# Kernel tuning notes

Hardware: AMD Instinct MI355X
Metric: run time of the kernel (lower is better)

Reference implementation:

```python
import jax, jax.numpy as jnp
import numpy as np

DIM = 1024
HEADS = 8
HD = DIM // HEADS          # 128
HALF = HD // 2             # 64 complex pairs
EPS = 1e-6
T, L, H, W = 10, 4, 21, 37
TOK_PER_FRAME = 1 + L * (5 + H * W)   # 3129
SK = T * TOK_PER_FRAME                # 31290
SQ = 512
THETA = 10000.0


def _inv_freqs(dim):
    # matches precompute_freqs_cis: 1/theta**(arange(0,dim,2)/dim)
    return 1.0 / THETA ** (np.arange(0, dim, 2)[: dim // 2].astype(np.float64) / dim)


def _angles(t_idx, h_idx, w_idx):
    # 3D RoPE split per precompute_freqs_cis_3d: f gets HD-2*(HD//3)=44 dims, h/w get HD//3=42 each
    hd3 = HD // 3
    inv_f = _inv_freqs(HD - 2 * hd3)  # 22 freqs
    inv_h = _inv_freqs(hd3)           # 21 freqs
    inv_w = _inv_freqs(hd3)           # 21 freqs
    ang = np.concatenate([
        t_idx[:, None] * inv_f[None, :],
        h_idx[:, None] * inv_h[None, :],
        w_idx[:, None] * inv_w[None, :],
    ], axis=-1)  # [S, 64]
    return ang


def _memory_positions():
    # per-frame layout from build_3d_freqs_unified: 1 pose token (h=w=0),
    # then per layer: 5 register tokens (h=w=0) + H*W grid tokens
    h_f, w_f = [0], [0]
    grid_h, grid_w = np.meshgrid(np.arange(H), np.arange(W), indexing='ij')
    for _ in range(L):
        h_f += [0] * 5 + list(grid_h.ravel())
        w_f += [0] * 5 + list(grid_w.ravel())
    h_f = np.asarray(h_f, np.float64)
    w_f = np.asarray(w_f, np.float64)
    t_idx = np.repeat(np.arange(T, dtype=np.float64), TOK_PER_FRAME)
    return t_idx, np.tile(h_f, T), np.tile(w_f, T)


def setup_inputs() -> dict:
    key = jax.random.key(0)
    ks = jax.random.split(key, 8)
    # RoPE angle tables
    tq = np.zeros(SQ)  # use_time_encoding=False for queries -> t=0
    hq = (np.arange(SQ) // W) % H
    wq = np.arange(SQ) % W
    ang_q = _angles(tq.astype(np.float64), hq.astype(np.float64), wq.astype(np.float64))
    tk, hk, wk = _memory_positions()
    ang_k = _angles(tk, hk, wk)
    s = 0.02
    inp = {
        'x': jax.random.normal(ks[0], (1, SQ, DIM), jnp.float32),
        'mem': jax.random.normal(ks[1], (1, SK, DIM), jnp.float32),
        'mask': jax.random.randint(ks[2], (1, SK), 0, 2) > 0,
        'cos_q': jnp.asarray(np.cos(ang_q), jnp.float32),
        'sin_q': jnp.asarray(np.sin(ang_q), jnp.float32),
        'cos_k': jnp.asarray(np.cos(ang_k), jnp.float32),
        'sin_k': jnp.asarray(np.sin(ang_k), jnp.float32),
        'Wq': jax.random.normal(ks[3], (DIM, DIM), jnp.float32) * s,
        'bq': jnp.zeros((DIM,), jnp.float32),
        'Wk': jax.random.normal(ks[4], (DIM, DIM), jnp.float32) * s,
        'bk': jnp.zeros((DIM,), jnp.float32),
        'Wv': jax.random.normal(ks[5], (DIM, DIM), jnp.float32) * s,
        'bv': jnp.zeros((DIM,), jnp.float32),
        'Wo': jax.random.normal(ks[6], (DIM, DIM), jnp.float32) * s,
        'bo': jnp.zeros((DIM,), jnp.float32),
        'gq': jnp.ones((DIM,), jnp.float32),
        'gk': jnp.ones((DIM,), jnp.float32),
    }
    return inp


def _rmsnorm(x, g):
    xf = x.astype(jnp.float32)
    y = xf * jax.lax.rsqrt(jnp.mean(xf * xf, axis=-1, keepdims=True) + EPS)
    return y.astype(x.dtype) * g


def _rope(x, cos, sin):
    # x: [B,S,D]; complex rotation on interleaved pairs per head, freqs shared across heads
    B, S, _ = x.shape
    xh = x.reshape(B, S, HEADS, HALF, 2)
    xr, xi = xh[..., 0], xh[..., 1]
    c = cos[None, :, None, :]
    s = sin[None, :, None, :]
    orr = xr * c - xi * s
    oi = xr * s + xi * c
    return jnp.stack([orr, oi], axis=-1).reshape(B, S, HEADS * HD)


def reference(x, mem, mask, cos_q, sin_q, cos_k, sin_k,
              Wq, bq, Wk, bk, Wv, bv, Wo, bo, gq, gk):
    q = _rmsnorm(x @ Wq.T + bq, gq)
    k = _rmsnorm(mem @ Wk.T + bk, gk)
    v = mem @ Wv.T + bv
    q = _rope(q, cos_q, sin_q)
    k = _rope(k, cos_k, sin_k)
    B, Sq, _ = q.shape
    Sk = k.shape[1]
    qh = q.reshape(B, Sq, HEADS, HD)
    kh = k.reshape(B, Sk, HEADS, HD)
    vh = v.reshape(B, Sk, HEADS, HD)
    scores = jnp.einsum('bqnd,bknd->bnqk', qh, kh) / jnp.sqrt(jnp.float32(HD))
    bias = jnp.where(mask[:, None, None, :], 0.0, -jnp.inf).astype(scores.dtype)
    attn = jax.nn.softmax(scores + bias, axis=-1)
    out = jnp.einsum('bnqk,bknd->bqnd', attn, vh).reshape(B, Sq, DIM)
    return out @ Wo.T + bo
```

## Files before the change

kernel.cpp:

```cpp
#include <hip/hip_runtime.h>
#include <cstdint>

typedef __bf16 bf16;
typedef __bf16 bf16x8 __attribute__((ext_vector_type(8)));
typedef __bf16 bf16x4 __attribute__((ext_vector_type(4)));
typedef float f32x4 __attribute__((ext_vector_type(4)));

#define DEVINL __device__ __forceinline__

namespace {
constexpr int DIM = 1024, HEADS = 8, HD = 128, HALF = 64;
constexpr int SQ = 512;
constexpr int SK = 31290;
constexpr int SKP = 31488;
constexpr int NSPLIT = 24;

constexpr long OFF_MEMB = 0;
constexpr long OFF_XB   = OFF_MEMB + (long)SKP * DIM * 2;
constexpr long OFF_WKV  = OFF_XB + (long)SQ * DIM * 2;
constexpr long OFF_WQ   = OFF_WKV + 2048L * DIM * 2;
constexpr long OFF_WO   = OFF_WQ + (long)DIM * DIM * 2;
constexpr long OFF_BKV  = OFF_WO + (long)DIM * DIM * 2;
constexpr long OFF_KPRE = OFF_BKV + 2048L * 4;
constexpr long OFF_VT   = OFF_KPRE + (long)SKP * DIM * 2;
constexpr long OFF_QPRE = OFF_VT + (long)DIM * SKP * 2;
constexpr long OFF_QR   = OFF_QPRE + (long)SQ * DIM * 4;
constexpr long OFF_BIAS = OFF_QR + (long)SQ * DIM * 2;
constexpr long OFF_ML   = OFF_BIAS + (long)SKP * 4;
constexpr long OFF_AO   = OFF_ML + (long)NSPLIT * HEADS * SQ * 2 * 4;
constexpr long OFF_IDX  = OFF_AO + (long)SQ * DIM * 2;
constexpr long OFF_NKC  = OFF_IDX + 31744L * 4;
constexpr long OFF_OP   = OFF_MEMB;
}

DEVINL void gl_lds16(const void* g, void* l) {
  __builtin_amdgcn_global_load_lds(
      (__attribute__((address_space(1))) void*)(void*)g,
      (__attribute__((address_space(3))) void*)l, 16, 0, 0);
}


__global__ __launch_bounds__(1024) void k_scan(const int* __restrict__ mask,
                                               int* __restrict__ idx,
                                               int* __restrict__ nkcp) {
  int tid = threadIdx.x, lane = tid & 63, wv = tid >> 6;
  __shared__ int wsum[16];
  __shared__ int base;
  if (tid == 0) base = 0;
  __syncthreads();
  for (int c = 0; c < 31; ++c) {
    int i = c * 1024 + tid;
    int m = (i < SK) ? (mask[i] != 0) : 0;
    unsigned long long bal = __ballot(m);
    int wpre = (int)__popcll(bal & ((1ull << lane) - 1ull));
    if (lane == 0) wsum[wv] = (int)__popcll(bal);
    __syncthreads();
    int woff = 0;
    #pragma unroll
    for (int j = 0; j < 16; ++j) woff += (j < wv) ? wsum[j] : 0;
    if (m) idx[base + woff + wpre] = i;
    __syncthreads();
    if (tid == 0) {
      int tot = 0;
      #pragma unroll
      for (int j = 0; j < 16; ++j) tot += wsum[j];
      base += tot;
    }
    __syncthreads();
  }
  if (tid == 0) *nkcp = base;
}


__global__ __launch_bounds__(256) void k_cvt_mem(const float* __restrict__ mem,
                                                 const int* __restrict__ idx,
                                                 const int* __restrict__ nkcp,
                                                 bf16* __restrict__ memb,
                                                 float* __restrict__ biasA) {
  long i = (long)blockIdx.x * 256 + threadIdx.x;
  long e = i * 8;
  if (e >= (long)SKP * DIM) return;
  int row = (int)(e >> 10);
  int nkc = *nkcp;
  int lim = ((((nkc + 63) & ~63) + 255) & ~255);
  if (row >= lim) return;
  if ((e & 1023) == 0) biasA[row] = (row < nkc) ? 0.0f : -1e30f;
  bf16x8 o;
  if (row < nkc) {
    long se = ((long)idx[row] << 10) + (e & 1023);
    float4 a = *(const float4*)(mem + se);
    float4 b = *(const float4*)(mem + se + 4);
    o[0] = (bf16)a.x; o[1] = (bf16)a.y; o[2] = (bf16)a.z; o[3] = (bf16)a.w;
    o[4] = (bf16)b.x; o[5] = (bf16)b.y; o[6] = (bf16)b.z; o[7] = (bf16)b.w;
  } else {
    #pragma unroll
    for (int j = 0; j < 8; ++j) o[j] = (bf16)0.0f;
  }
  *(bf16x8*)(memb + e) = o;
}

__global__ __launch_bounds__(256) void k_prep(const float* __restrict__ x,
    const float* __restrict__ Wq, const float* __restrict__ Wo,
    const float* __restrict__ Wk, const float* __restrict__ Wv,
    const float* __restrict__ bk, const float* __restrict__ bv,
    bf16* __restrict__ xb, bf16* __restrict__ WqB, bf16* __restrict__ WoB,
    bf16* __restrict__ WkvB, float* __restrict__ bKV) {
  long i = (long)blockIdx.x * 256 + threadIdx.x;
  constexpr long n_x = 65536, n_w = 131072;
  const float* src;
  bf16* dst;
  long off;
  if (i < n_x) { src = x; dst = xb; off = i; }
  else if (i < n_x + n_w) { src = Wq; dst = WqB; off = i - n_x; }
  else if (i < n_x + 2 * n_w) { src = Wo; dst = WoB; off = i - n_x - n_w; }
  else if (i < n_x + 2 * n_w + 262144) {
    long j = i - n_x - 2 * n_w;
    long e = j * 8;
    int n = (int)(e >> 10);
    const float* s2 = (n < 1024) ? (Wk + e) : (Wv + e - 1024L * 1024);
    float4 a = *(const float4*)(s2);
    float4 b = *(const float4*)(s2 + 4);
    bf16x8 o;
    o[0] = (bf16)a.x; o[1] = (bf16)a.y; o[2] = (bf16)a.z; o[3] = (bf16)a.w;
    o[4] = (bf16)b.x; o[5] = (bf16)b.y; o[6] = (bf16)b.z; o[7] = (bf16)b.w;
    *(bf16x8*)(WkvB + e) = o;
    if (j < 2048) bKV[j] = (j < 1024) ? bk[j] : bv[j - 1024];
    return;
  } else return;
  long e = off * 8;
  float4 a = *(const float4*)(src + e);
  float4 b = *(const float4*)(src + e + 4);
  bf16x8 o;
  o[0] = (bf16)a.x; o[1] = (bf16)a.y; o[2] = (bf16)a.z; o[3] = (bf16)a.w;
  o[4] = (bf16)b.x; o[5] = (bf16)b.y; o[6] = (bf16)b.z; o[7] = (bf16)b.w;
  *(bf16x8*)(dst + e) = o;
}


template<int MODE>
__global__ __launch_bounds__(256, 2)
void k_gemm(const bf16* __restrict__ A, const bf16* __restrict__ B,
            const float* __restrict__ bias, int Mtiles, int Ntiles,
            float* __restrict__ outF, int ldF,
            bf16* __restrict__ outK, bf16* __restrict__ outVT) {
  constexpr int K = 1024;
  __shared__ char lds[32768];
  char* ldsA = lds;
  char* ldsB = lds + 16384;
  int tid = threadIdx.x;
  int w = tid >> 6, lane = tid & 63;
  int cpx = gridDim.x >> 3;
  int bid = (blockIdx.x & 7) * cpx + (blockIdx.x >> 3);
  int mt = bid / Ntiles, nt = bid % Ntiles;
  int m0 = mt * 128, n0 = nt * 128;
  int wm = w >> 1, wn = w & 1;
  int cl = lane & 15, rg = lane >> 4;

  f32x4 acc[4][4] = {};

  int rowi = lane >> 3, g = lane & 7;
  for (int kt = 0; kt < K / 64; ++kt) {
    #pragma unroll
    for (int j = 0; j < 4; ++j) {
      int rb = (w * 4 + j) * 8;
      int row = rb + rowi;
      int gs = g ^ (row & 7);
      gl_lds16((const char*)(A + (long)(m0 + row) * K + kt * 64) + gs * 16, ldsA + rb * 128);
      gl_lds16((const char*)(B + (long)(n0 + row) * K + kt * 64) + gs * 16, ldsB + rb * 128);
    }
    __syncthreads();
    #pragma unroll
    for (int ks = 0; ks < 2; ++ks) {
      bf16x8 af[4], bfr[4];
      #pragma unroll
      for (int i = 0; i < 4; ++i) {
        int rowA = wm * 64 + i * 16 + cl;
        int c = ks * 4 + rg;
        af[i] = *(const bf16x8*)(ldsA + rowA * 128 + ((c ^ (rowA & 7)) * 16));
        int rowB = wn * 64 + i * 16 + cl;
        bfr[i] = *(const bf16x8*)(ldsB + rowB * 128 + ((c ^ (rowB & 7)) * 16));
      }
      #pragma unroll
      for (int mf = 0; mf < 4; ++mf)
        #pragma unroll
        for (int nf = 0; nf < 4; ++nf)
          acc[mf][nf] = __builtin_amdgcn_mfma_f32_16x16x32_bf16(af[mf], bfr[nf], acc[mf][nf], 0, 0, 0);
    }
    __syncthreads();
  }

  #pragma unroll
  for (int mf = 0; mf < 4; ++mf) {
    #pragma unroll
    for (int nf = 0; nf < 4; ++nf) {
      int n = n0 + wn * 64 + nf * 16 + cl;
      float bval = bias[n];
      int mb = m0 + wm * 64 + mf * 16 + rg * 4;
      #pragma unroll
      for (int rr = 0; rr < 4; ++rr)
        outF[(long)(mb + rr) * ldF + n] = acc[mf][nf][rr] + bval;
    }
  }
}


#define KV_PHASE(P)                                                                   \
  {                                                                                   \
    bf16x8 a00 = dsA(cur, 2 * (P), 0),     a01 = dsA(cur, 2 * (P), 1);                \
    bf16x8 a10 = dsA(cur, 2 * (P) + 1, 0), a11 = dsA(cur, 2 * (P) + 1, 1);            \
    __builtin_amdgcn_s_setprio(1);                                                    \
    _Pragma("unroll")                                                                 \
    for (int nf = 0; nf < 4; ++nf) {                                                  \
      acc[2 * (P)][nf]     = __builtin_amdgcn_mfma_f32_16x16x32_bf16(a00, bb[nf][0], acc[2 * (P)][nf], 0, 0, 0);     \
      acc[2 * (P) + 1][nf] = __builtin_amdgcn_mfma_f32_16x16x32_bf16(a10, bb[nf][0], acc[2 * (P) + 1][nf], 0, 0, 0); \
    }                                                                                 \
    _Pragma("unroll")                                                                 \
    for (int nf = 0; nf < 4; ++nf) {                                                  \
      acc[2 * (P)][nf]     = __builtin_amdgcn_mfma_f32_16x16x32_bf16(a01, bb[nf][1], acc[2 * (P)][nf], 0, 0, 0);     \
      acc[2 * (P) + 1][nf] = __builtin_amdgcn_mfma_f32_16x16x32_bf16(a11, bb[nf][1], acc[2 * (P) + 1][nf], 0, 0, 0); \
    }                                                                                 \
    __builtin_amdgcn_s_setprio(0);                                                    \
  }

__global__ __launch_bounds__(512)
void k_gemm_kv(const bf16* __restrict__ A, const bf16* __restrict__ B,
               const float* __restrict__ bias, const int* __restrict__ nkcp,
               bf16* __restrict__ outK, bf16* __restrict__ outVT) {
  constexpr int K = 1024, NTK = 16;
  __shared__ char lds[131072];
  const int tid = threadIdx.x;
  const int w = tid >> 6, lane = tid & 63;
  const int mt = blockIdx.x >> 3, nt = blockIdx.x & 7;
  const int m0 = mt * 256, n0 = nt * 256;
  if (m0 >= ((*nkcp + 63) & ~63)) return;
  const int wm = w >> 2, wn = w & 3;
  const int cl = lane & 15, rg = lane >> 4;
  const int srow = lane >> 3, sg = lane & 7;

  f32x4 acc[8][4] = {};

  auto stage = [&](int b, int kt, int isB, int cr) {
    const bf16* src = isB ? B : A;
    int r = cr + w * 8 + srow;
    int gs = sg ^ (r & 7);
    const char* gp = (const char*)(src + (long)((isB ? n0 : m0) + r) * K + kt * 64) + gs * 16;
    char* lp = lds + b * 65536 + isB * 32768 + (cr + w * 8) * 128;
    gl_lds16(gp, lp);
  };
  auto dsA = [&](int b, int mf, int ks) -> bf16x8 {
    int r = wm * 128 + mf * 16 + cl;
    int c = ks * 4 + rg;
    return *(const bf16x8*)(lds + b * 65536 + r * 128 + ((c ^ (r & 7)) * 16));
  };
  auto dsB = [&](int b, int nf, int ks) -> bf16x8 {
    int r = wn * 64 + nf * 16 + cl;
    int c = ks * 4 + rg;
    return *(const bf16x8*)(lds + b * 65536 + 32768 + r * 128 + ((c ^ (r & 7)) * 16));
  };

  stage(0, 0, 1, 0);   stage(0, 0, 1, 64);
  stage(0, 0, 1, 128); stage(0, 0, 1, 192);
  stage(0, 0, 0, 0);   stage(0, 0, 0, 128);
  stage(0, 0, 0, 64);  stage(0, 0, 0, 192);

  for (int t = 0; t < NTK; ++t) {
    const int cur = t & 1, nxt = cur ^ 1;
    const bool pre = (t + 1 < NTK);
    bf16x8 bb[4][2];

    if (pre) {
      stage(nxt, t + 1, 1, 0); stage(nxt, t + 1, 1, 64);
      asm volatile("s_waitcnt vmcnt(4)\ns_barrier" ::: "memory");
    } else {
      asm volatile("s_waitcnt vmcnt(2)\ns_barrier" ::: "memory");
    }
    #pragma unroll
    for (int nf = 0; nf < 4; ++nf) { bb[nf][0] = dsB(cur, nf, 0); bb[nf][1] = dsB(cur, nf, 1); }
    KV_PHASE(0)
    asm volatile("s_barrier" ::: "memory");
    if (pre) { stage(nxt, t + 1, 1, 128); stage(nxt, t + 1, 1, 192); }
    KV_PHASE(1)
    asm volatile("s_barrier" ::: "memory");
    if (pre) {
      stage(nxt, t + 1, 0, 0); stage(nxt, t + 1, 0, 128);
      asm volatile("s_waitcnt vmcnt(6)\ns_barrier" ::: "memory");
    } else {
      asm volatile("s_waitcnt vmcnt(0)\ns_barrier" ::: "memory");
    }
    KV_PHASE(2)
    asm volatile("s_barrier" ::: "memory");
    if (pre) { stage(nxt, t + 1, 0, 64); stage(nxt, t + 1, 0, 192); }
    KV_PHASE(3)
    asm volatile("s_barrier" ::: "memory");
  }

  if (nt < 4) {
    #pragma unroll
    for (int mf = 0; mf < 8; ++mf)
      #pragma unroll
      for (int nf = 0; nf < 4; ++nf) {
        int n = n0 + wn * 64 + nf * 16 + cl;
        float bval = bias[n];
        int mrow = m0 + wm * 128 + mf * 16 + rg * 4;
        #pragma unroll
        for (int rr = 0; rr < 4; ++rr)
          outK[(long)(mrow + rr) * 1024 + n] = (bf16)(acc[mf][nf][rr] + bval);
      }
  } else {
    #pragma unroll
    for (int mf = 0; mf < 8; ++mf)
      #pragma unroll
      for (int nf = 0; nf < 4; ++nf) {
        int n = n0 + wn * 64 + nf * 16 + cl;
        float bval = bias[n];
        int mrow = m0 + wm * 128 + mf * 16 + rg * 4;
        bf16x4 pk;
        #pragma unroll
        for (int rr = 0; rr < 4; ++rr) pk[rr] = (bf16)(acc[mf][nf][rr] + bval);
        *(bf16x4*)(outVT + (long)(n - 1024) * SKP + mrow) = pk;
      }
  }
}


__global__ __launch_bounds__(256) void k_fuse_q(const float* __restrict__ QP,
    bf16* __restrict__ Qr, const float* __restrict__ gg,
    const float* __restrict__ cosT, const float* __restrict__ sinT) {
  int row = blockIdx.x, tid = threadIdx.x;
  int d0 = tid * 4;
  float4 t = *(const float4*)(QP + (long)row * DIM + d0);
  float v0 = t.x, v1 = t.y, v2 = t.z, v3 = t.w;
  float ss = v0 * v0 + v1 * v1 + v2 * v2 + v3 * v3;
  #pragma unroll
  for (int m = 1; m < 64; m <<= 1) ss += __shfl_xor(ss, m);
  __shared__ float red[4];
  if ((tid & 63) == 0) red[tid >> 6] = ss;
  __syncthreads();
  float rn = rsqrtf((red[0] + red[1] + red[2] + red[3]) * (1.0f / DIM) + 1e-6f);
  v0 *= rn * gg[d0]; v1 *= rn * gg[d0 + 1]; v2 *= rn * gg[d0 + 2]; v3 *= rn * gg[d0 + 3];
  int i0 = (d0 & 127) >> 1;
  float c0 = cosT[(long)row * HALF + i0], s0 = sinT[(long)row * HALF + i0];
  float c1 = cosT[(long)row * HALF + i0 + 1], s1 = sinT[(long)row * HALF + i0 + 1];
  bf16x4 o = { (bf16)(v0 * c0 - v1 * s0), (bf16)(v0 * s0 + v1 * c0),
               (bf16)(v2 * c1 - v3 * s1), (bf16)(v2 * s1 + v3 * c1) };
  *(bf16x4*)(Qr + (long)row * DIM + d0) = o;
}

__global__ __launch_bounds__(256) void k_fuse_k(bf16* __restrict__ KP,
    const float* __restrict__ gg, const float* __restrict__ cosT,
    const float* __restrict__ sinT, const int* __restrict__ idx,
    const int* __restrict__ nkcp) {
  int row = blockIdx.x, tid = threadIdx.x;
  int nkc = *nkcp;
  if (row >= ((nkc + 63) & ~63)) return;
  int orig = (row < nkc) ? idx[row] : 0;
  int d0 = tid * 4;
  bf16x4 t = *(const bf16x4*)(KP + (long)row * DIM + d0);
  float v0 = (float)t[0], v1 = (float)t[1], v2 = (float)t[2], v3 = (float)t[3];
  float ss = v0 * v0 + v1 * v1 + v2 * v2 + v3 * v3;
  #pragma unroll
  for (int m = 1; m < 64; m <<= 1) ss += __shfl_xor(ss, m);
  __shared__ float red[4];
  if ((tid & 63) == 0) red[tid >> 6] = ss;
  __syncthreads();
  float rn = rsqrtf((red[0] + red[1] + red[2] + red[3]) * (1.0f / DIM) + 1e-6f);
  v0 *= rn * gg[d0]; v1 *= rn * gg[d0 + 1]; v2 *= rn * gg[d0 + 2]; v3 *= rn * gg[d0 + 3];
  int i0 = (d0 & 127) >> 1;
  float c0 = cosT[(long)orig * HALF + i0], s0 = sinT[(long)orig * HALF + i0];
  float c1 = cosT[(long)orig * HALF + i0 + 1], s1 = sinT[(long)orig * HALF + i0 + 1];
  bf16x4 o = { (bf16)(v0 * c0 - v1 * s0), (bf16)(v0 * s0 + v1 * c0),
               (bf16)(v2 * c1 - v3 * s1), (bf16)(v2 * s1 + v3 * c1) };
  *(bf16x4*)(KP + (long)row * DIM + d0) = o;
}


__global__ __launch_bounds__(256, 2)
void k_attn(const bf16* __restrict__ Kr, const bf16* __restrict__ VT,
            const bf16* __restrict__ Qr, const float* __restrict__ biasA,
            const int* __restrict__ nkcp,
            float* __restrict__ Opart, float* __restrict__ ml) {
  __shared__ char lds[49152];
  char* ldsK = lds;
  char* ldsV = lds + 16384;
  int tid = threadIdx.x, w = tid >> 6, lane = tid & 63;
  char* ldsP = lds + 32768 + w * 4096;
  int bid = blockIdx.x;
  int swz = (bid & 7) * 96 + (bid >> 3);
  int sp = swz >> 5, h = (swz >> 2) & 7, qb = swz & 3;
  int NTC = (*nkcp + 63) >> 6;
  int t0 = (sp * NTC) / NSPLIT;
  int t1 = ((sp + 1) * NTC) / NSPLIT;
  int cl = lane & 15, rg = lane >> 4;
  int qbase = qb * 128 + w * 32;

  bf16x8 qf[2][4];
  #pragma unroll
  for (int mf = 0; mf < 2; ++mf)
    #pragma unroll
    for (int ks = 0; ks < 4; ++ks)
      qf[mf][ks] = *(const bf16x8*)(Qr + (long)(qbase + mf * 16 + cl) * DIM + h * HD + ks * 32 + rg * 8);

  bf16x8 ones;
  #pragma unroll
  for (int j = 0; j < 8; ++j) ones[j] = (bf16)1.0f;

  f32x4 Oa[2][8] = {};
  f32x4 l_acc[2] = {};
  float m_r[2] = {-1e30f, -1e30f};

  const float sc = 0.08838834764831845f;
  for (int t = t0; t < t1; ++t) {
    int k0 = t * 64;
    __syncthreads();
    {
      int rK = lane >> 4, gK = lane & 15;
      #pragma unroll
      for (int j = 0; j < 4; ++j) {
        int rb = w * 16 + j * 4;
        int row = rb + rK;
        int gs = gK ^ (row & 7);
        gl_lds16((const char*)(Kr + (long)(k0 + row) * DIM + h * HD) + gs * 16,
                 ldsK + rb * 256);
      }
      int rV = lane >> 3, gV = lane & 7;
      #pragma unroll
      for (int j = 0; j < 4; ++j) {
        int db = w * 32 + j * 8;
        int d = db + rV;
        int gs = gV ^ (d & 7);
        gl_lds16((const char*)(VT + (long)(h * HD + d) * SKP + k0) + gs * 16,
                 ldsV + db * 128);
      }
    }
    __syncthreads();

    f32x4 sa[2][4] = {};
    #pragma unroll
    for (int ks = 0; ks < 4; ++ks) {
      #pragma unroll
      for (int nf = 0; nf < 4; ++nf) {
        int key = nf * 16 + cl;
        int c = ks * 4 + rg;
        bf16x8 kb = *(const bf16x8*)(ldsK + key * 256 + ((c ^ (key & 7)) * 16));
        sa[0][nf] = __builtin_amdgcn_mfma_f32_16x16x32_bf16(qf[0][ks], kb, sa[0][nf], 0, 0, 0);
        sa[1][nf] = __builtin_amdgcn_mfma_f32_16x16x32_bf16(qf[1][ks], kb, sa[1][nf], 0, 0, 0);
      }
    }

    float bia[4];
    #pragma unroll
    for (int nf = 0; nf < 4; ++nf) bia[nf] = biasA[k0 + nf * 16 + cl];

    #pragma unroll
    for (int mf = 0; mf < 2; ++mf) {
      char* ldsPmf = ldsP + mf * 2048;
      #pragma unroll
      for (int nf = 0; nf < 4; ++nf)
        #pragma unroll
        for (int r = 0; r < 4; ++r) sa[mf][nf][r] = sa[mf][nf][r] * sc + bia[nf];
      float mx = sa[mf][0][0];
      #pragma unroll
      for (int nf = 0; nf < 4; ++nf)
        #pragma unroll
        for (int r = 0; r < 4; ++r) mx = fmaxf(mx, sa[mf][nf][r]);
      mx = fmaxf(mx, __shfl_xor(mx, 1));
      mx = fmaxf(mx, __shfl_xor(mx, 2));
      mx = fmaxf(mx, __shfl_xor(mx, 4));
      mx = fmaxf(mx, __shfl_xor(mx, 8));
      bool grew = mx > m_r[mf] + 6.0f;
      if (__any(grew)) {
        float mn = grew ? mx : m_r[mf];
        float scale = __expf(m_r[mf] - mn);
        m_r[mf] = mn;
        l_acc[mf] *= scale;
        #pragma unroll
        for (int df = 0; df < 8; ++df) Oa[mf][df] *= scale;
      }
      #pragma unroll
      for (int nf = 0; nf < 4; ++nf)
        #pragma unroll
        for (int r = 0; r < 4; ++r) {
          float p = __expf(sa[mf][nf][r] - m_r[mf]);
          int qr = rg * 4 + r;
          int col = nf * 16 + cl;
          int gp = (col >> 3) ^ (qr & 7);
          *(bf16*)(ldsPmf + qr * 128 + gp * 16 + (col & 7) * 2) = (bf16)p;
        }
    }

    #pragma unroll
    for (int ks = 0; ks < 2; ++ks) {
      int c = ks * 4 + rg;
      bf16x8 pa0 = *(const bf16x8*)(ldsP + cl * 128 + ((c ^ (cl & 7)) * 16));
      bf16x8 pa1 = *(const bf16x8*)(ldsP + 2048 + cl * 128 + ((c ^ (cl & 7)) * 16));
      l_acc[0] = __builtin_amdgcn_mfma_f32_16x16x32_bf16(pa0, ones, l_acc[0], 0, 0, 0);
      l_acc[1] = __builtin_amdgcn_mfma_f32_16x16x32_bf16(pa1, ones, l_acc[1], 0, 0, 0);
      #pragma unroll
      for (int df = 0; df < 8; ++df) {
        int d = df * 16 + cl;
        bf16x8 vb = *(const bf16x8*)(ldsV + d * 128 + ((c ^ (d & 7)) * 16));
        Oa[0][df] = __builtin_amdgcn_mfma_f32_16x16x32_bf16(pa0, vb, Oa[0][df], 0, 0, 0);
        Oa[1][df] = __builtin_amdgcn_mfma_f32_16x16x32_bf16(pa1, vb, Oa[1][df], 0, 0, 0);
      }
    }
  }

  long rowb = (long)(sp * HEADS + h) * SQ + qbase;
  #pragma unroll
  for (int mf = 0; mf < 2; ++mf) {
    #pragma unroll
    for (int df = 0; df < 8; ++df)
      #pragma unroll
      for (int r = 0; r < 4; ++r) {
        int qr = mf * 16 + rg * 4 + r;
        Opart[(rowb + qr) * HD + df * 16 + cl] = Oa[mf][df][r];
      }
    if (cl == 0) {
      #pragma unroll
      for (int r = 0; r < 4; ++r) {
        int qr = mf * 16 + rg * 4 + r;
        ml[(rowb + qr) * 2] = m_r[mf];
        ml[(rowb + qr) * 2 + 1] = l_acc[mf][r];
      }
    }
  }
}

__global__ __launch_bounds__(128) void k_combine(const float* __restrict__ Opart,
    const float* __restrict__ ml, bf16* __restrict__ AO) {
  int bid = blockIdx.x;
  int h = bid >> 9, qq = bid & 511;
  int d = threadIdx.x;
  float M = -1e30f;
  #pragma unroll 4
  for (int s2 = 0; s2 < NSPLIT; ++s2) {
    long mi = (long)(s2 * HEADS + h) * SQ + qq;
    M = fmaxf(M, ml[mi * 2]);
  }
  float L = 0.f, acc = 0.f;
  #pragma unroll 4
  for (int s2 = 0; s2 < NSPLIT; ++s2) {
    long mi = (long)(s2 * HEADS + h) * SQ + qq;
    float wgt = __expf(ml[mi * 2] - M);
    L += wgt * ml[mi * 2 + 1];
    acc += wgt * Opart[mi * HD + d];
  }
  AO[(long)qq * DIM + h * HD + d] = (bf16)(acc / L);
}


extern "C" void kernel_launch(void* const* d_in, const int* in_sizes, int n_in,
                              void* d_out, int out_size, void* d_ws, size_t ws_size,
                              hipStream_t stream) {
  const float* x     = (const float*)d_in[0];
  const float* mem   = (const float*)d_in[1];
  const int*   mask  = (const int*)d_in[2];
  const float* cos_q = (const float*)d_in[3];
  const float* sin_q = (const float*)d_in[4];
  const float* cos_k = (const float*)d_in[5];
  const float* sin_k = (const float*)d_in[6];
  const float* Wq    = (const float*)d_in[7];
  const float* bq    = (const float*)d_in[8];
  const float* Wk    = (const float*)d_in[9];
  const float* bk    = (const float*)d_in[10];
  const float* Wv    = (const float*)d_in[11];
  const float* bv    = (const float*)d_in[12];
  const float* Wo    = (const float*)d_in[13];
  const float* bo    = (const float*)d_in[14];
  const float* gq    = (const float*)d_in[15];
  const float* gk    = (const float*)d_in[16];

  char* ws = (char*)d_ws;
  bf16*  memb = (bf16*)(ws + OFF_MEMB);
  bf16*  xb   = (bf16*)(ws + OFF_XB);
  bf16*  WkvB = (bf16*)(ws + OFF_WKV);
  bf16*  WqB  = (bf16*)(ws + OFF_WQ);
  bf16*  WoB  = (bf16*)(ws + OFF_WO);
  float* bKV  = (float*)(ws + OFF_BKV);
  bf16*  Kpre = (bf16*)(ws + OFF_KPRE);
  bf16*  VT   = (bf16*)(ws + OFF_VT);
  float* Qpre = (float*)(ws + OFF_QPRE);
  bf16*  Qr   = (bf16*)(ws + OFF_QR);
  float* biasA= (float*)(ws + OFF_BIAS);
  float* Opart= (float*)(ws + OFF_OP);
  float* mlb  = (float*)(ws + OFF_ML);
  bf16*  AO   = (bf16*)(ws + OFF_AO);
  int*   idx  = (int*)(ws + OFF_IDX);
  int*   nkcp = (int*)(ws + OFF_NKC);

  k_scan<<<dim3(1), dim3(1024), 0, stream>>>(mask, idx, nkcp);
  k_cvt_mem<<<dim3(SKP * DIM / 8 / 256), dim3(256), 0, stream>>>(mem, idx, nkcp, memb, biasA);
  k_prep<<<dim3(2304), dim3(256), 0, stream>>>(x, Wq, Wo, Wk, Wv, bk, bv,
                                               xb, WqB, WoB, WkvB, bKV);

  k_gemm<0><<<dim3(4 * 8), dim3(256), 0, stream>>>(xb, WqB, bq, 4, 8, Qpre, DIM,
                                                   (bf16*)nullptr, (bf16*)nullptr);
  k_gemm_kv<<<dim3(984), dim3(512), 0, stream>>>(memb, WkvB, bKV, nkcp, Kpre, VT);

  k_fuse_q<<<dim3(SQ), dim3(256), 0, stream>>>(Qpre, Qr, gq, cos_q, sin_q);
  k_fuse_k<<<dim3(SKP), dim3(256), 0, stream>>>(Kpre, gk, cos_k, sin_k, idx, nkcp);

  k_attn<<<dim3(NSPLIT * HEADS * 4), dim3(256), 0, stream>>>(Kpre, VT, Qr, biasA, nkcp, Opart, mlb);
  k_combine<<<dim3(HEADS * SQ), dim3(128), 0, stream>>>(Opart, mlb, AO);

  k_gemm<0><<<dim3(4 * 8), dim3(256), 0, stream>>>(AO, WoB, bo, 4, 8, (float*)d_out, DIM,
                                                   (bf16*)nullptr, (bf16*)nullptr);
  (void)in_sizes; (void)n_in; (void)out_size; (void)ws_size;
}
```

Measured before the change: 257.1 us.

## Transpose QK MFMA so softmax rows are lane-local; drop bias buffer and ones-MFMA

The score MFMA now has its operands swapped so each lane holds keys for a fixed query, which cuts the row max/sum reductions to two cross-lane shuffles instead of four. The row sum is accumulated in registers, which removes the extra MFMA against a vector of ones. The key mask is computed inline from nkc, so the bias buffer and its global loads go away. Each P tile is stored in row-major LDS with a 144-byte padded stride instead of an XOR swizzle. In exchange, rescaling the output accumulator now needs per-row scale shuffles, and LDS use per block grows slightly.

```diff
diff --git a/kernel.cpp b/kernel.cpp
--- a/kernel.cpp
+++ b/kernel.cpp
@@ -25,8 +25,7 @@
 constexpr long OFF_VT   = OFF_KPRE + (long)SKP * DIM * 2;
 constexpr long OFF_QPRE = OFF_VT + (long)DIM * SKP * 2;
 constexpr long OFF_QR   = OFF_QPRE + (long)SQ * DIM * 4;
-constexpr long OFF_BIAS = OFF_QR + (long)SQ * DIM * 2;
-constexpr long OFF_ML   = OFF_BIAS + (long)SKP * 4;
+constexpr long OFF_ML   = OFF_QR + (long)SQ * DIM * 2;
 constexpr long OFF_AO   = OFF_ML + (long)NSPLIT * HEADS * SQ * 2 * 4;
 constexpr long OFF_IDX  = OFF_AO + (long)SQ * DIM * 2;
 constexpr long OFF_NKC  = OFF_IDX + 31744L * 4;
@@ -75,8 +74,7 @@
 __global__ __launch_bounds__(256) void k_cvt_mem(const float* __restrict__ mem,
                                                  const int* __restrict__ idx,
                                                  const int* __restrict__ nkcp,
-                                                 bf16* __restrict__ memb,
-                                                 float* __restrict__ biasA) {
+                                                 bf16* __restrict__ memb) {
   long i = (long)blockIdx.x * 256 + threadIdx.x;
   long e = i * 8;
   if (e >= (long)SKP * DIM) return;
@@ -84,7 +82,6 @@
   int nkc = *nkcp;
   int lim = ((((nkc + 63) & ~63) + 255) & ~255);
   if (row >= lim) return;
-  if ((e & 1023) == 0) biasA[row] = (row < nkc) ? 0.0f : -1e30f;
   bf16x8 o;
   if (row < nkc) {
     long se = ((long)idx[row] << 10) + (e & 1023);
@@ -376,18 +373,18 @@
 
 __global__ __launch_bounds__(256, 2)
 void k_attn(const bf16* __restrict__ Kr, const bf16* __restrict__ VT,
-            const bf16* __restrict__ Qr, const float* __restrict__ biasA,
-            const int* __restrict__ nkcp,
+            const bf16* __restrict__ Qr, const int* __restrict__ nkcp,
             float* __restrict__ Opart, float* __restrict__ ml) {
-  __shared__ char lds[49152];
+  __shared__ char lds[51200];
   char* ldsK = lds;
   char* ldsV = lds + 16384;
   int tid = threadIdx.x, w = tid >> 6, lane = tid & 63;
-  char* ldsP = lds + 32768 + w * 4096;
+  char* ldsP = lds + 32768 + w * 4608;
   int bid = blockIdx.x;
   int swz = (bid & 7) * 96 + (bid >> 3);
   int sp = swz >> 5, h = (swz >> 2) & 7, qb = swz & 3;
-  int NTC = (*nkcp + 63) >> 6;
+  int nkc = *nkcp;
+  int NTC = (nkc + 63) >> 6;
   int t0 = (sp * NTC) / NSPLIT;
   int t1 = ((sp + 1) * NTC) / NSPLIT;
   int cl = lane & 15, rg = lane >> 4;
@@ -400,13 +397,9 @@
     for (int ks = 0; ks < 4; ++ks)
       qf[mf][ks] = *(const bf16x8*)(Qr + (long)(qbase + mf * 16 + cl) * DIM + h * HD + ks * 32 + rg * 8);
 
-  bf16x8 ones;
-  #pragma unroll
-  for (int j = 0; j < 8; ++j) ones[j] = (bf16)1.0f;
-
   f32x4 Oa[2][8] = {};
-  f32x4 l_acc[2] = {};
   float m_r[2] = {-1e30f, -1e30f};
+  float l_r[2] = {0.f, 0.f};
 
   const float sc = 0.08838834764831845f;
   for (int t = t0; t < t1; ++t) {
@@ -442,59 +435,70 @@
         int key = nf * 16 + cl;
         int c = ks * 4 + rg;
         bf16x8 kb = *(const bf16x8*)(ldsK + key * 256 + ((c ^ (key & 7)) * 16));
-        sa[0][nf] = __builtin_amdgcn_mfma_f32_16x16x32_bf16(qf[0][ks], kb, sa[0][nf], 0, 0, 0);
-        sa[1][nf] = __builtin_amdgcn_mfma_f32_16x16x32_bf16(qf[1][ks], kb, sa[1][nf], 0, 0, 0);
-      }
-    }
-
-    float bia[4];
-    #pragma unroll
-    for (int nf = 0; nf < 4; ++nf) bia[nf] = biasA[k0 + nf * 16 + cl];
+        sa[0][nf] = __builtin_amdgcn_mfma_f32_16x16x32_bf16(kb, qf[0][ks], sa[0][nf], 0, 0, 0);
+        sa[1][nf] = __builtin_amdgcn_mfma_f32_16x16x32_bf16(kb, qf[1][ks], sa[1][nf], 0, 0, 0);
+      }
+    }
 
     #pragma unroll
     for (int mf = 0; mf < 2; ++mf) {
-      char* ldsPmf = ldsP + mf * 2048;
       #pragma unroll
       for (int nf = 0; nf < 4; ++nf)
         #pragma unroll
-        for (int r = 0; r < 4; ++r) sa[mf][nf][r] = sa[mf][nf][r] * sc + bia[nf];
+        for (int r = 0; r < 4; ++r) {
+          int key = k0 + nf * 16 + rg * 4 + r;
+          sa[mf][nf][r] = (key < nkc) ? sa[mf][nf][r] * sc : -1e30f;
+        }
       float mx = sa[mf][0][0];
       #pragma unroll
       for (int nf = 0; nf < 4; ++nf)
         #pragma unroll
         for (int r = 0; r < 4; ++r) mx = fmaxf(mx, sa[mf][nf][r]);
-      mx = fmaxf(mx, __shfl_xor(mx, 1));
-      mx = fmaxf(mx, __shfl_xor(mx, 2));
-      mx = fmaxf(mx, __shfl_xor(mx, 4));
-      mx = fmaxf(mx, __shfl_xor(mx, 8));
+      mx = fmaxf(mx, __shfl_xor(mx, 16));
+      mx = fmaxf(mx, __shfl_xor(mx, 32));
       bool grew = mx > m_r[mf] + 6.0f;
       if (__any(grew)) {
         float mn = grew ? mx : m_r[mf];
-        float scale = __expf(m_r[mf] - mn);
+        float scl = __expf(m_r[mf] - mn);
         m_r[mf] = mn;
-        l_acc[mf] *= scale;
+        l_r[mf] *= scl;
+        int sb = lane & 48;
+        float s0 = __shfl(scl, sb | (rg * 4 + 0));
+        float s1 = __shfl(scl, sb | (rg * 4 + 1));
+        float s2 = __shfl(scl, sb | (rg * 4 + 2));
+        float s3 = __shfl(scl, sb | (rg * 4 + 3));
         #pragma unroll
-        for (int df = 0; df < 8; ++df) Oa[mf][df] *= scale;
-      }
+        for (int df = 0; df < 8; ++df) {
+          Oa[mf][df][0] *= s0; Oa[mf][df][1] *= s1;
+          Oa[mf][df][2] *= s2; Oa[mf][df][3] *= s3;
+        }
+      }
+      float rsum = 0.f;
       #pragma unroll
       for (int nf = 0; nf < 4; ++nf)
         #pragma unroll
         for (int r = 0; r < 4; ++r) {
           float p = __expf(sa[mf][nf][r] - m_r[mf]);
-          int qr = rg * 4 + r;
-          int col = nf * 16 + cl;
-          int gp = (col >> 3) ^ (qr & 7);
-          *(bf16*)(ldsPmf + qr * 128 + gp * 16 + (col & 7) * 2) = (bf16)p;
+          sa[mf][nf][r] = p;
+          rsum += p;
         }
+      rsum += __shfl_xor(rsum, 16);
+      rsum += __shfl_xor(rsum, 32);
+      l_r[mf] += rsum;
+      char* prow = ldsP + (mf * 16 + cl) * 144;
+      #pragma unroll
+      for (int nf = 0; nf < 4; ++nf) {
+        bf16x4 pk = { (bf16)sa[mf][nf][0], (bf16)sa[mf][nf][1],
+                      (bf16)sa[mf][nf][2], (bf16)sa[mf][nf][3] };
+        *(bf16x4*)(prow + nf * 32 + rg * 8) = pk;
+      }
     }
 
     #pragma unroll
     for (int ks = 0; ks < 2; ++ks) {
+      bf16x8 pa0 = *(const bf16x8*)(ldsP + cl * 144 + ks * 64 + rg * 16);
+      bf16x8 pa1 = *(const bf16x8*)(ldsP + (16 + cl) * 144 + ks * 64 + rg * 16);
       int c = ks * 4 + rg;
-      bf16x8 pa0 = *(const bf16x8*)(ldsP + cl * 128 + ((c ^ (cl & 7)) * 16));
-      bf16x8 pa1 = *(const bf16x8*)(ldsP + 2048 + cl * 128 + ((c ^ (cl & 7)) * 16));
-      l_acc[0] = __builtin_amdgcn_mfma_f32_16x16x32_bf16(pa0, ones, l_acc[0], 0, 0, 0);
-      l_acc[1] = __builtin_amdgcn_mfma_f32_16x16x32_bf16(pa1, ones, l_acc[1], 0, 0, 0);
       #pragma unroll
       for (int df = 0; df < 8; ++df) {
         int d = df * 16 + cl;
@@ -515,13 +519,12 @@
         int qr = mf * 16 + rg * 4 + r;
         Opart[(rowb + qr) * HD + df * 16 + cl] = Oa[mf][df][r];
       }
-    if (cl == 0) {
-      #pragma unroll
-      for (int r = 0; r < 4; ++r) {
-        int qr = mf * 16 + rg * 4 + r;
-        ml[(rowb + qr) * 2] = m_r[mf];
-        ml[(rowb + qr) * 2 + 1] = l_acc[mf][r];
-      }
+  }
+  if (rg == 0) {
+    #pragma unroll
+    for (int mf = 0; mf < 2; ++mf) {
+      ml[(rowb + mf * 16 + cl) * 2] = m_r[mf];
+      ml[(rowb + mf * 16 + cl) * 2 + 1] = l_r[mf];
     }
   }
 }
@@ -581,7 +584,6 @@
   bf16*  VT   = (bf16*)(ws + OFF_VT);
   float* Qpre = (float*)(ws + OFF_QPRE);
   bf16*  Qr   = (bf16*)(ws + OFF_QR);
-  float* biasA= (float*)(ws + OFF_BIAS);
   float* Opart= (float*)(ws + OFF_OP);
   float* mlb  = (float*)(ws + OFF_ML);
   bf16*  AO   = (bf16*)(ws + OFF_AO);
@@ -589,7 +591,7 @@
   int*   nkcp = (int*)(ws + OFF_NKC);
 
   k_scan<<<dim3(1), dim3(1024), 0, stream>>>(mask, idx, nkcp);
-  k_cvt_mem<<<dim3(SKP * DIM / 8 / 256), dim3(256), 0, stream>>>(mem, idx, nkcp, memb, biasA);
+  k_cvt_mem<<<dim3(SKP * DIM / 8 / 256), dim3(256), 0, stream>>>(mem, idx, nkcp, memb);
   k_prep<<<dim3(2304), dim3(256), 0, stream>>>(x, Wq, Wo, Wk, Wv, bk, bv,
                                                xb, WqB, WoB, WkvB, bKV);
 
@@ -600,7 +602,7 @@
   k_fuse_q<<<dim3(SQ), dim3(256), 0, stream>>>(Qpre, Qr, gq, cos_q, sin_q);
   k_fuse_k<<<dim3(SKP), dim3(256), 0, stream>>>(Kpre, gk, cos_k, sin_k, idx, nkcp);
 
-  k_attn<<<dim3(NSPLIT * HEADS * 4), dim3(256), 0, stream>>>(Kpre, VT, Qr, biasA, nkcp, Opart, mlb);
+  k_attn<<<dim3(NSPLIT * HEADS * 4), dim3(256), 0, stream>>>(Kpre, VT, Qr, nkcp, Opart, mlb);
   k_combine<<<dim3(HEADS * SQ), dim3(128), 0, stream>>>(Opart, mlb, AO);
 
   k_gemm<0><<<dim3(4 * 8), dim3(256), 0, stream>>>(AO, WoB, bo, 4, 8, (float*)d_out, DIM,
```

Result: no change. 255.4 us (-0.7%).
